# Optimization experiments

Measured on AMD Instinct MI355X. Metric: run time of the kernel, lower is better.

The kernel has to match this reference:

```python
import jax, jax.numpy as jnp
import numpy as np

V, E, H, L, B, S = 32000, 256, 512, 2, 128, 512


def _lstm_step(x, h, c, w_ih, w_hh, b_ih, b_hh):
    # PyTorch gate order: i, f, g, o
    gates = x @ w_ih.T + b_ih + h @ w_hh.T + b_hh
    i, f, g, o = jnp.split(gates, 4, axis=-1)
    c2 = jax.nn.sigmoid(f) * c + jax.nn.sigmoid(i) * jnp.tanh(g)
    h2 = jax.nn.sigmoid(o) * jnp.tanh(c2)
    return h2, c2


def setup_inputs() -> dict:
    key = jax.random.key(0)
    ks = jax.random.split(key, 16)
    s = 0.05
    d = {}
    d["dec_input"] = jax.random.randint(ks[0], (B,), 0, V)
    d["hidden"] = jax.random.normal(ks[1], (L, B, H), jnp.float32)
    d["cell"] = jax.random.normal(ks[2], (L, B, H), jnp.float32)
    d["encoder_outputs"] = jax.random.normal(ks[3], (S, B, H), jnp.float32)
    d["emb"] = jax.random.normal(ks[4], (V, E), jnp.float32) * s
    d["attn_w"] = jax.random.normal(ks[5], (1, 2 * H), jnp.float32) * s
    d["attn_b"] = jnp.zeros((1,), jnp.float32)
    d["w_ih0"] = jax.random.normal(ks[6], (4 * H, E + H), jnp.float32) * s
    d["w_hh0"] = jax.random.normal(ks[7], (4 * H, H), jnp.float32) * s
    d["b_ih0"] = jnp.zeros((4 * H,), jnp.float32)
    d["b_hh0"] = jnp.zeros((4 * H,), jnp.float32)
    d["w_ih1"] = jax.random.normal(ks[8], (4 * H, H), jnp.float32) * s
    d["w_hh1"] = jax.random.normal(ks[9], (4 * H, H), jnp.float32) * s
    d["b_ih1"] = jnp.zeros((4 * H,), jnp.float32)
    d["b_hh1"] = jnp.zeros((4 * H,), jnp.float32)
    d["fc_w"] = jax.random.normal(ks[10], (V, H), jnp.float32) * s
    d["fc_b"] = jnp.zeros((V,), jnp.float32)
    return d


def reference(dec_input, hidden, cell, encoder_outputs, emb, attn_w, attn_b,
              w_ih0, w_hh0, b_ih0, b_hh0, w_ih1, w_hh1, b_ih1, b_hh1,
              fc_w, fc_b):
    # embedded: [B, E]  (dropout p=0 -> identity)
    embedded = emb[dec_input]
    # Bahdanau-style additive scoring using FIRST-layer hidden (as in source)
    h0 = hidden[0]                                   # [B, H]
    w_enc, w_hid = attn_w[0, :H], attn_w[0, H:]      # split linear over concat
    # logits[b,s] = enc[s,b]@w_enc + h0[b]@w_hid + b
    logits = jnp.einsum('sbh,h->bs', encoder_outputs, w_enc) \
        + (h0 @ w_hid)[:, None] + attn_b[0]          # [B, S]
    alpha = jax.nn.softmax(logits, axis=1)           # softmax over src positions
    # context = sum_s alpha[b,s] * enc[s,b,:]  (avoids repeat_interleave blowup)
    context = jnp.einsum('bs,sbh->bh', alpha, encoder_outputs)  # [B, H]
    x = jnp.concatenate([context, embedded], axis=1)            # [B, H+E]
    # single-timestep 2-layer LSTM
    h_0, c_0 = _lstm_step(x, hidden[0], cell[0], w_ih0, w_hh0, b_ih0, b_hh0)
    h_1, c_1 = _lstm_step(h_0, hidden[1], cell[1], w_ih1, w_hh1, b_ih1, b_hh1)
    new_hidden = jnp.stack([h_0, h_1])
    new_cell = jnp.stack([c_0, c_1])
    prediction = h_1 @ fc_w.T + fc_b                 # [B, V]
    return prediction, new_hidden, new_cell
```

## Files before the change

kernel.cpp:

```cpp
#include <hip/hip_runtime.h>
#include <hip/hip_bf16.h>
#include <math.h>

constexpr int NV = 32000;
constexpr int NE = 256;
constexpr int NH = 512;
constexpr int NB = 128;
constexpr int NS = 512;
constexpr int NX = NH + NE;
constexpr int NSC = 8;

typedef __attribute__((ext_vector_type(8))) short short8;
typedef __attribute__((ext_vector_type(4))) short short4v;
typedef __attribute__((ext_vector_type(4))) float f32x4;

constexpr size_t OFF_PCTX  = 0;
constexpr size_t OFF_PML   = OFF_PCTX  + (size_t)NB*NSC*NH;
constexpr size_t OFF_XBF   = OFF_PML   + (size_t)NB*NSC*2;
constexpr size_t OFF_H0NBF = OFF_XBF   + 49152;
constexpr size_t OFF_H1NBF = OFF_H0NBF + 32768;
constexpr size_t OFF_H0BFI = OFF_H1NBF + 32768;
constexpr size_t OFF_H1BFI = OFF_H0BFI + 32768;

constexpr size_t OUT_HID  = (size_t)NB * NV;
constexpr size_t OUT_CELL = OUT_HID + 2ull * NB * NH;

__device__ inline float sigf(float x) { return 1.0f / (1.0f + expf(-x)); }
__device__ inline short bf16s(float x) {
  __hip_bfloat16 h = __float2bfloat16(x);
  return *reinterpret_cast<short*>(&h);
}

__global__ __launch_bounds__(256) void attn_partial_k(
    const float* __restrict__ enc, const float* __restrict__ attn_w,
    float* __restrict__ pctx, float* __restrict__ pml) {
  const int sc = blockIdx.x, b = blockIdx.y;
  const int wv = threadIdx.x >> 6, lane = threadIdx.x & 63;
  const f32x4 wa = *reinterpret_cast<const f32x4*>(attn_w + lane * 4);
  const f32x4 wb = *reinterpret_cast<const f32x4*>(attn_w + 256 + lane * 4);
  float m0 = -INFINITY, l0 = 0.f, m1 = -INFINITY, l1 = 0.f;
  f32x4 a00 = {}, a01 = {}, a10 = {}, a11 = {};
  const float* base = enc + ((size_t)(sc * 64 + wv) * NB + b) * NH;
  for (int i = 0; i < 8; ++i) {
    const float* r0 = base + (size_t)(i * 4) * NB * NH;
    const float* r1 = base + (size_t)((i + 8) * 4) * NB * NH;
    f32x4 e00 = *reinterpret_cast<const f32x4*>(r0 + lane * 4);
    f32x4 e01 = *reinterpret_cast<const f32x4*>(r0 + 256 + lane * 4);
    f32x4 e10 = *reinterpret_cast<const f32x4*>(r1 + lane * 4);
    f32x4 e11 = *reinterpret_cast<const f32x4*>(r1 + 256 + lane * 4);
    float d0 = e00.x * wa.x + e00.y * wa.y + e00.z * wa.z + e00.w * wa.w
             + e01.x * wb.x + e01.y * wb.y + e01.z * wb.z + e01.w * wb.w;
    float d1 = e10.x * wa.x + e10.y * wa.y + e10.z * wa.z + e10.w * wa.w
             + e11.x * wb.x + e11.y * wb.y + e11.z * wb.z + e11.w * wb.w;
#pragma unroll
    for (int off = 32; off; off >>= 1) {
      d0 += __shfl_xor(d0, off);
      d1 += __shfl_xor(d1, off);
    }
    float mn0 = fmaxf(m0, d0), mn1 = fmaxf(m1, d1);
    float s0 = expf(m0 - mn0), s1 = expf(m1 - mn1);
    float p0 = expf(d0 - mn0), p1 = expf(d1 - mn1);
    l0 = l0 * s0 + p0;         l1 = l1 * s1 + p1;
    a00 = a00 * s0 + p0 * e00; a01 = a01 * s0 + p0 * e01;
    a10 = a10 * s1 + p1 * e10; a11 = a11 * s1 + p1 * e11;
    m0 = mn0; m1 = mn1;
  }
  const float Mw = fmaxf(m0, m1);
  const float c0 = expf(m0 - Mw), c1 = expf(m1 - Mw);
  const float lw = l0 * c0 + l1 * c1;
  const f32x4 accA = a00 * c0 + a10 * c1;
  const f32x4 accB = a01 * c0 + a11 * c1;
  __shared__ float sm[4], sl[4], sacc[4][NH];
  if (lane == 0) { sm[wv] = Mw; sl[wv] = lw; }
  *reinterpret_cast<f32x4*>(&sacc[wv][lane * 4]) = accA;
  *reinterpret_cast<f32x4*>(&sacc[wv][256 + lane * 4]) = accB;
  __syncthreads();
  const float M = fmaxf(fmaxf(sm[0], sm[1]), fmaxf(sm[2], sm[3]));
  const float e0 = expf(sm[0] - M), e1 = expf(sm[1] - M),
              e2 = expf(sm[2] - M), e3 = expf(sm[3] - M);
  const int t = threadIdx.x;
  float* outc = pctx + ((size_t)b * NSC + sc) * NH;
#pragma unroll
  for (int q = 0; q < 2; ++q) {
    int h = q * 256 + t;
    outc[h] = sacc[0][h] * e0 + sacc[1][h] * e1 + sacc[2][h] * e2 + sacc[3][h] * e3;
  }
  if (t == 0) {
    pml[((size_t)b * NSC + sc) * 2 + 0] = M;
    pml[((size_t)b * NSC + sc) * 2 + 1] = sl[0] * e0 + sl[1] * e1 + sl[2] * e2 + sl[3] * e3;
  }
}

__global__ __launch_bounds__(256) void attn_finish_k(
    const float* __restrict__ pctx, const float* __restrict__ pml,
    const float* __restrict__ emb, const int* __restrict__ dec,
    const float* __restrict__ hidden,
    __hip_bfloat16* __restrict__ xbf,
    __hip_bfloat16* __restrict__ h0bf, __hip_bfloat16* __restrict__ h1bf) {
  const int b = blockIdx.x, t = threadIdx.x;
  float ms[NSC];
  float M = -INFINITY;
#pragma unroll
  for (int sc = 0; sc < NSC; ++sc) {
    ms[sc] = pml[((size_t)b * NSC + sc) * 2 + 0];
    M = fmaxf(M, ms[sc]);
  }
  float L = 0.f, es[NSC];
#pragma unroll
  for (int sc = 0; sc < NSC; ++sc) {
    es[sc] = expf(ms[sc] - M);
    L += pml[((size_t)b * NSC + sc) * 2 + 1] * es[sc];
  }
  const float invL = 1.f / L;
#pragma unroll
  for (int q = 0; q < 2; ++q) {
    int h = q * 256 + t;
    float v = 0.f;
#pragma unroll
    for (int sc = 0; sc < NSC; ++sc)
      v += pctx[((size_t)b * NSC + sc) * NH + h] * es[sc];
    xbf[(size_t)b * NX + h] = __float2bfloat16(v * invL);
    h0bf[(size_t)b * NH + h] = __float2bfloat16(hidden[(size_t)b * NH + h]);
    h1bf[(size_t)b * NH + h] =
        __float2bfloat16(hidden[(size_t)(NB * NH) + (size_t)b * NH + h]);
  }
  xbf[(size_t)b * NX + NH + t] = __float2bfloat16(emb[(size_t)dec[b] * NE + t]);
}

constexpr int LSLAB = 520;
template <int KX>
__global__ __launch_bounds__(128, 2) void lstm_fused_k(
    const float* __restrict__ Wx, const float* __restrict__ Wh,
    const __hip_bfloat16* __restrict__ Ax, const __hip_bfloat16* __restrict__ Ah,
    const float* __restrict__ b_ih, const float* __restrict__ b_hh,
    const float* __restrict__ c_in,
    float* __restrict__ h_out, float* __restrict__ c_out,
    __hip_bfloat16* __restrict__ hbf_out) {
  constexpr int NCHX = KX / 256;
  constexpr int NCH = NCHX + 2;
  __shared__ short wlds[2][8 * LSLAB];
  __shared__ float sg[32][17];
  const int tid = threadIdx.x, wv = tid >> 6, lane = tid & 63;
  const int l15 = lane & 15, lhi = lane >> 4;
  const int mh = blockIdx.x, p = blockIdx.y;
  const int srow = tid >> 6;
  const int scol = lane * 4;
  const int soff0 = (scol >> 5) * LSLAB + (scol & 31);
  const int arow = mh * 32 + wv * 16 + l15;

  short8 afbuf[2][8];
  f32x4 wr[8];

#define A_LOAD(c, buf)                                                        \
  {                                                                           \
    const __hip_bfloat16* ab =                                                \
        ((c) < NCHX) ? (Ax + (size_t)arow * KX + (c) * 256 + lhi * 8)         \
                     : (Ah + (size_t)arow * NH + ((c) - NCHX) * 256 + lhi * 8);\
    _Pragma("unroll")                                                         \
    for (int ks = 0; ks < 8; ++ks)                                            \
      (buf)[ks] = *reinterpret_cast<const short8*>(ab + ks * 32);             \
  }
#define LSTAGE_LOAD(c)                                                        \
  {                                                                           \
    const bool fx = (c) < NCHX;                                               \
    const float* Ws = fx ? Wx : Wh;                                           \
    const int Ks = fx ? KX : NH;                                              \
    const int cb = fx ? (c) * 256 : ((c) - NCHX) * 256;                       \
    _Pragma("unroll")                                                         \
    for (int i = 0; i < 8; ++i) {                                             \
      const int j = i * 2 + srow;                                             \
      const int g = j >> 2, rr = j & 3;                                       \
      wr[i] = *reinterpret_cast<const f32x4*>(                                \
          Ws + (size_t)(g * NH + p * 4 + rr) * Ks + cb + scol);               \
    }                                                                         \
  }
#define LSTAGE_WRITE(buf)                                                     \
  {                                                                           \
    _Pragma("unroll")                                                         \
    for (int i = 0; i < 8; ++i) {                                             \
      const int j = i * 2 + srow;                                             \
      short4v cv;                                                             \
      cv[0] = bf16s(wr[i].x); cv[1] = bf16s(wr[i].y);                         \
      cv[2] = bf16s(wr[i].z); cv[3] = bf16s(wr[i].w);                         \
      *reinterpret_cast<short4v*>((buf) + soff0 + j * 32) = cv;               \
    }                                                                         \
  }

  A_LOAD(0, afbuf[0]);
  LSTAGE_LOAD(0);
  LSTAGE_WRITE(wlds[0]);
  __syncthreads();

  f32x4 acc = {};
#pragma unroll
  for (int c = 0; c < NCH; ++c) {
    if (c + 1 < NCH) {
      LSTAGE_LOAD(c + 1);
      A_LOAD(c + 1, afbuf[(c + 1) & 1]);
    }
    {
      const short* wb = wlds[c & 1];
#pragma unroll
      for (int ks = 0; ks < 8; ++ks) {
        short8 bf = *reinterpret_cast<const short8*>(wb + ks * LSLAB + l15 * 32 + lhi * 8);
        acc = __builtin_amdgcn_mfma_f32_16x16x32_bf16(afbuf[c & 1][ks], bf, acc, 0, 0, 0);
      }
    }
    if (c + 1 < NCH) {
      LSTAGE_WRITE(wlds[(c + 1) & 1]);
      __syncthreads();
    }
  }
#pragma unroll
  for (int q = 0; q < 4; ++q)
    sg[wv * 16 + lhi * 4 + q][l15] = acc[q];
  __syncthreads();
  {
    const int bl = tid >> 2, r = tid & 3;
    const int b = mh * 32 + bl;
    const int h = p * 4 + r;
    float ig = sg[bl][0 + r]  + b_ih[0 * NH + h] + b_hh[0 * NH + h];
    float fg = sg[bl][4 + r]  + b_ih[1 * NH + h] + b_hh[1 * NH + h];
    float gg = sg[bl][8 + r]  + b_ih[2 * NH + h] + b_hh[2 * NH + h];
    float og = sg[bl][12 + r] + b_ih[3 * NH + h] + b_hh[3 * NH + h];
    float c = c_in[(size_t)b * NH + h];
    float c2 = sigf(fg) * c + sigf(ig) * tanhf(gg);
    float h2 = sigf(og) * tanhf(c2);
    c_out[(size_t)b * NH + h] = c2;
    h_out[(size_t)b * NH + h] = h2;
    hbf_out[(size_t)b * NH + h] = __float2bfloat16(h2);
  }
#undef A_LOAD
#undef LSTAGE_LOAD
#undef LSTAGE_WRITE
}

constexpr int FC_PANELS = 8;
constexpr int FC_BLOCKS = NV / (16 * FC_PANELS);
constexpr int SLAB = 520;

__global__ __launch_bounds__(256, 1) void gemm_fc_pipe_k(
    const __hip_bfloat16* __restrict__ Abf, const float* __restrict__ W,
    const float* __restrict__ bias, float* __restrict__ out) {
  __shared__ short wlds[3][16 * SLAB];
  const int tid = threadIdx.x, wv = tid >> 6, lane = tid & 63;
  const int l15 = lane & 15, lhi = lane >> 4;
  const int nbase = blockIdx.x * (16 * FC_PANELS);

  int soff[8];
#pragma unroll
  for (int i = 0; i < 8; ++i) {
    const int o = i * 1024 + tid * 4;
    const int n = o >> 9, kk = o & 511;
    soff[i] = (kk >> 5) * SLAB + n * 32 + (kk & 31);
  }

  short8 af[2][16];
#pragma unroll
  for (int m = 0; m < 2; ++m) {
    const __hip_bfloat16* ar = Abf + (size_t)(wv * 32 + m * 16 + l15) * NH + lhi * 8;
#pragma unroll
    for (int ks = 0; ks < 16; ++ks)
      af[m][ks] = *reinterpret_cast<const short8*>(ar + ks * 32);
  }

  f32x4 wrb[2][8];
  {
    const float* p0 = W + (size_t)nbase * NH;
#pragma unroll
    for (int i = 0; i < 8; ++i)
      wrb[0][i] = *reinterpret_cast<const f32x4*>(p0 + i * 1024 + tid * 4);
    const float* p1 = W + (size_t)(nbase + 16) * NH;
#pragma unroll
    for (int i = 0; i < 8; ++i)
      wrb[1][i] = *reinterpret_cast<const f32x4*>(p1 + i * 1024 + tid * 4);
#pragma unroll
    for (int i = 0; i < 8; ++i) {
      short4v cv;
      cv[0] = bf16s(wrb[0][i].x); cv[1] = bf16s(wrb[0][i].y);
      cv[2] = bf16s(wrb[0][i].z); cv[3] = bf16s(wrb[0][i].w);
      *reinterpret_cast<short4v*>(wlds[0] + soff[i]) = cv;
    }
  }
  __syncthreads();

  f32x4 s0 = {}, s1 = {};
  int sn0 = -1;
#pragma unroll
  for (int p = 0; p < FC_PANELS; ++p) {
    if (p + 2 < FC_PANELS) {
      const float* pan = W + (size_t)(nbase + (p + 2) * 16) * NH;
#pragma unroll
      for (int i = 0; i < 8; ++i)
        wrb[p & 1][i] = *reinterpret_cast<const f32x4*>(pan + i * 1024 + tid * 4);
    }
    if (sn0 >= 0) {
      const float bv = bias[sn0 + l15];
#pragma unroll
      for (int q = 0; q < 4; ++q) {
        out[(size_t)(wv * 32 + 0 * 16 + lhi * 4 + q) * NV + sn0 + l15] = s0[q] + bv;
        out[(size_t)(wv * 32 + 1 * 16 + lhi * 4 + q) * NV + sn0 + l15] = s1[q] + bv;
      }
    }
    if (p + 1 < FC_PANELS) {
      short* dst = wlds[(p + 1) % 3];
#pragma unroll
      for (int i = 0; i < 8; ++i) {
        short4v cv;
        cv[0] = bf16s(wrb[(p + 1) & 1][i].x); cv[1] = bf16s(wrb[(p + 1) & 1][i].y);
        cv[2] = bf16s(wrb[(p + 1) & 1][i].z); cv[3] = bf16s(wrb[(p + 1) & 1][i].w);
        *reinterpret_cast<short4v*>(dst + soff[i]) = cv;
      }
    }
    {
      const short* wb = wlds[p % 3];
      f32x4 a0 = {}, a1 = {};
#pragma unroll
      for (int ks = 0; ks < 16; ++ks) {
        short8 bf = *reinterpret_cast<const short8*>(wb + ks * SLAB + l15 * 32 + lhi * 8);
        a0 = __builtin_amdgcn_mfma_f32_16x16x32_bf16(af[0][ks], bf, a0, 0, 0, 0);
        a1 = __builtin_amdgcn_mfma_f32_16x16x32_bf16(af[1][ks], bf, a1, 0, 0, 0);
      }
      s0 = a0; s1 = a1; sn0 = nbase + p * 16;
    }
    __syncthreads();
  }
  {
    const float bv = bias[sn0 + l15];
#pragma unroll
    for (int q = 0; q < 4; ++q) {
      out[(size_t)(wv * 32 + 0 * 16 + lhi * 4 + q) * NV + sn0 + l15] = s0[q] + bv;
      out[(size_t)(wv * 32 + 1 * 16 + lhi * 4 + q) * NV + sn0 + l15] = s1[q] + bv;
    }
  }
}

extern "C" void kernel_launch(void* const* d_in, const int* in_sizes, int n_in,
                              void* d_out, int out_size, void* d_ws, size_t ws_size,
                              hipStream_t stream) {
  const int*   dec    = (const int*)d_in[0];
  const float* hidden = (const float*)d_in[1];
  const float* cell   = (const float*)d_in[2];
  const float* enc    = (const float*)d_in[3];
  const float* emb    = (const float*)d_in[4];
  const float* attn_w = (const float*)d_in[5];
  const float* w_ih0  = (const float*)d_in[7];
  const float* w_hh0  = (const float*)d_in[8];
  const float* b_ih0  = (const float*)d_in[9];
  const float* b_hh0  = (const float*)d_in[10];
  const float* w_ih1  = (const float*)d_in[11];
  const float* w_hh1  = (const float*)d_in[12];
  const float* b_ih1  = (const float*)d_in[13];
  const float* b_hh1  = (const float*)d_in[14];
  const float* fc_w   = (const float*)d_in[15];
  const float* fc_b   = (const float*)d_in[16];
  float* out = (float*)d_out;
  float* ws  = (float*)d_ws;

  float* pctx = ws + OFF_PCTX;
  float* pml  = ws + OFF_PML;
  __hip_bfloat16* xbf   = (__hip_bfloat16*)(ws + OFF_XBF);
  __hip_bfloat16* h0nbf = (__hip_bfloat16*)(ws + OFF_H0NBF);
  __hip_bfloat16* h1nbf = (__hip_bfloat16*)(ws + OFF_H1NBF);
  __hip_bfloat16* h0bf  = (__hip_bfloat16*)(ws + OFF_H0BFI);
  __hip_bfloat16* h1bf  = (__hip_bfloat16*)(ws + OFF_H1BFI);

  attn_partial_k<<<dim3(NSC, NB), 256, 0, stream>>>(enc, attn_w, pctx, pml);
  attn_finish_k<<<NB, 256, 0, stream>>>(pctx, pml, emb, dec, hidden,
                                        xbf, h0bf, h1bf);
  lstm_fused_k<NX><<<dim3(4, NH / 4), 128, 0, stream>>>(
      w_ih0, w_hh0, xbf, h0bf, b_ih0, b_hh0, cell,
      out + OUT_HID, out + OUT_CELL, h0nbf);
  lstm_fused_k<NH><<<dim3(4, NH / 4), 128, 0, stream>>>(
      w_ih1, w_hh1, h0nbf, h1bf, b_ih1, b_hh1, cell + NB * NH,
      out + OUT_HID + (size_t)NB * NH,
      out + OUT_CELL + (size_t)NB * NH, h1nbf);
  gemm_fc_pipe_k<<<FC_BLOCKS, 256, 0, stream>>>(h1nbf, fc_w, fc_b, out);
}
```

Before: 65.56 us.

## Deepen LSTM gate GEMM pipeline to prefetch two chunks ahead

The LSTM fused kernel now loads weights and activations two chunks ahead into register buffers and keeps a triple-buffered LDS ring. The bf16 conversion and LDS write for the next chunk happen before the MFMA loop on the current chunk instead of after it. The aim is to hide global load latency better within a short pipeline. The cost is more registers (an extra A buffer and weight buffer) and more LDS, which may lower occupancy under launch_bounds(128,2).

```diff
diff --git a/kernel.cpp b/kernel.cpp
--- a/kernel.cpp
+++ b/kernel.cpp
@@ -138,7 +138,7 @@
     __hip_bfloat16* __restrict__ hbf_out) {
   constexpr int NCHX = KX / 256;
   constexpr int NCH = NCHX + 2;
-  __shared__ short wlds[2][8 * LSLAB];
+  __shared__ short wlds[3][8 * LSLAB];
   __shared__ float sg[32][17];
   const int tid = threadIdx.x, wv = tid >> 6, lane = tid & 63;
   const int l15 = lane & 15, lhi = lane >> 4;
@@ -148,8 +148,8 @@
   const int soff0 = (scol >> 5) * LSLAB + (scol & 31);
   const int arow = mh * 32 + wv * 16 + l15;
 
-  short8 afbuf[2][8];
-  f32x4 wr[8];
+  short8 abuf[3][8];
+  f32x4 wrb[2][8];
 
 #define A_LOAD(c, buf)                                                        \
   {                                                                           \
@@ -160,7 +160,7 @@
     for (int ks = 0; ks < 8; ++ks)                                            \
       (buf)[ks] = *reinterpret_cast<const short8*>(ab + ks * 32);             \
   }
-#define LSTAGE_LOAD(c)                                                        \
+#define W_LOAD(c, buf)                                                        \
   {                                                                           \
     const bool fx = (c) < NCHX;                                               \
     const float* Ws = fx ? Wx : Wh;                                           \
@@ -170,46 +170,45 @@
     for (int i = 0; i < 8; ++i) {                                             \
       const int j = i * 2 + srow;                                             \
       const int g = j >> 2, rr = j & 3;                                       \
-      wr[i] = *reinterpret_cast<const f32x4*>(                                \
+      (buf)[i] = *reinterpret_cast<const f32x4*>(                             \
           Ws + (size_t)(g * NH + p * 4 + rr) * Ks + cb + scol);               \
     }                                                                         \
   }
-#define LSTAGE_WRITE(buf)                                                     \
+#define W_CONV(buf, dst)                                                      \
   {                                                                           \
     _Pragma("unroll")                                                         \
     for (int i = 0; i < 8; ++i) {                                             \
       const int j = i * 2 + srow;                                             \
       short4v cv;                                                             \
-      cv[0] = bf16s(wr[i].x); cv[1] = bf16s(wr[i].y);                         \
-      cv[2] = bf16s(wr[i].z); cv[3] = bf16s(wr[i].w);                         \
-      *reinterpret_cast<short4v*>((buf) + soff0 + j * 32) = cv;               \
+      cv[0] = bf16s((buf)[i].x); cv[1] = bf16s((buf)[i].y);                   \
+      cv[2] = bf16s((buf)[i].z); cv[3] = bf16s((buf)[i].w);                   \
+      *reinterpret_cast<short4v*>((dst) + soff0 + j * 32) = cv;               \
     }                                                                         \
   }
 
-  A_LOAD(0, afbuf[0]);
-  LSTAGE_LOAD(0);
-  LSTAGE_WRITE(wlds[0]);
+  W_LOAD(0, wrb[0]); A_LOAD(0, abuf[0]);
+  W_LOAD(1, wrb[1]); A_LOAD(1, abuf[1]);
+  W_CONV(wrb[0], wlds[0]);
   __syncthreads();
 
   f32x4 acc = {};
 #pragma unroll
   for (int c = 0; c < NCH; ++c) {
-    if (c + 1 < NCH) {
-      LSTAGE_LOAD(c + 1);
-      A_LOAD(c + 1, afbuf[(c + 1) & 1]);
-    }
+    if (c + 2 < NCH) {
+      W_LOAD(c + 2, wrb[c & 1]);
+      A_LOAD(c + 2, abuf[(c + 2) % 3]);
+    }
+    if (c + 1 < NCH)
+      W_CONV(wrb[(c + 1) & 1], wlds[(c + 1) % 3]);
     {
-      const short* wb = wlds[c & 1];
+      const short* wb = wlds[c % 3];
 #pragma unroll
       for (int ks = 0; ks < 8; ++ks) {
         short8 bf = *reinterpret_cast<const short8*>(wb + ks * LSLAB + l15 * 32 + lhi * 8);
-        acc = __builtin_amdgcn_mfma_f32_16x16x32_bf16(afbuf[c & 1][ks], bf, acc, 0, 0, 0);
+        acc = __builtin_amdgcn_mfma_f32_16x16x32_bf16(abuf[c % 3][ks], bf, acc, 0, 0, 0);
       }
     }
-    if (c + 1 < NCH) {
-      LSTAGE_WRITE(wlds[(c + 1) & 1]);
-      __syncthreads();
-    }
+    __syncthreads();
   }
 #pragma unroll
   for (int q = 0; q < 4; ++q)
@@ -231,8 +230,8 @@
     hbf_out[(size_t)b * NH + h] = __float2bfloat16(h2);
   }
 #undef A_LOAD
-#undef LSTAGE_LOAD
-#undef LSTAGE_WRITE
+#undef W_LOAD
+#undef W_CONV
 }
 
 constexpr int FC_PANELS = 8;
```

After: 65.95 us. Within noise of the previous version (+0.6%).
